# Kernel tuning notes

Measured on AMD Instinct MI355X. Metric: run time of the kernel, lower is better.

The kernel has to match this reference:

```python
import jax, jax.numpy as jnp
import numpy as np

B, C, N = 4, 256, 4096
C4 = C // 4  # q/k projection dim (channels // 4)
BN_EPS = 1e-5


def setup_inputs() -> dict:
    key = jax.random.key(0)
    ks = jax.random.split(key, 4)
    s = 0.05
    return {
        "x": jax.random.normal(ks[0], (B, C, N), jnp.float32),
        # q_conv and k_conv share this weight in the original module
        "wq": jax.random.normal(ks[1], (C4, C), jnp.float32) * s,
        "wv": jax.random.normal(ks[2], (C, C), jnp.float32) * s,
        "bv": jnp.zeros((C,), jnp.float32),
        "wt": jax.random.normal(ks[3], (C, C), jnp.float32) * s,
        "bt": jnp.zeros((C,), jnp.float32),
        "gamma": jnp.ones((C,), jnp.float32),
        "beta": jnp.zeros((C,), jnp.float32),
        "running_mean": jnp.zeros((C,), jnp.float32),
        "running_var": jnp.ones((C,), jnp.float32),
    }


def reference(x, wq, wv, bv, wt, bt, gamma, beta, running_mean, running_var):
    # 1x1 Conv1d == channel matmul. q/k share wq.
    q = jnp.einsum('oc,bcn->bno', wq, x)            # [B, N, C4]
    k = jnp.einsum('oc,bcn->bon', wq, x)            # [B, C4, N]
    energy = jnp.einsum('bno,bom->bnm', q, k)       # [B, N, N]
    attn = jax.nn.softmax(energy, axis=-1)
    # offset-attention L1 re-normalization over dim 1 (query axis)
    attn = attn / (1e-9 + attn.sum(axis=1, keepdims=True))
    v = jnp.einsum('oc,bcn->bon', wv, x) + bv[None, :, None]   # [B, C, N]
    # x_r[b,c,n] = sum_m v[b,c,m] * attn[b,n,m]
    x_r = jnp.einsum('bcm,bnm->bcn', v, attn)       # [B, C, N]
    t = jnp.einsum('oc,bcn->bon', wt, x - x_r) + bt[None, :, None]
    # BatchNorm1d in inference mode (running stats)
    inv = jax.lax.rsqrt(running_var + BN_EPS)
    bn = (t - running_mean[None, :, None]) * (gamma * inv)[None, :, None] + beta[None, :, None]
    return x + jax.nn.relu(bn)
```

## Files before the change

### kernel.cpp

```cpp
#include <hip/hip_runtime.h>
#include <math.h>

namespace {

constexpr int B_ = 4;
constexpr int C_ = 256;
constexpr int C4_ = 64;
constexpr int N_ = 4096;

typedef __attribute__((ext_vector_type(8))) short bf16x8;
typedef __attribute__((ext_vector_type(4))) float f32x4;

__device__ __forceinline__ unsigned short bf16_rne(float f) {
    unsigned u = __float_as_uint(f);
    u += 0x7fffu + ((u >> 16) & 1u);
    return (unsigned short)(u >> 16);
}

__device__ __forceinline__ void g2l16(const unsigned short* g, unsigned short* l) {
    __builtin_amdgcn_global_load_lds(
        (const __attribute__((address_space(1))) unsigned int*)g,
        (__attribute__((address_space(3))) unsigned int*)l, 16, 0, 0);
}

__global__ __launch_bounds__(256) void cvt_kernel(
        const float* __restrict__ wq, const float* __restrict__ wv,
        const float* __restrict__ wt, unsigned short* __restrict__ wcomb,
        unsigned short* __restrict__ wtb) {
    const int i = (blockIdx.x * 256 + threadIdx.x) * 4;
    const float* src;
    unsigned short* dst;
    if (i < 16384) { src = wq + i; dst = wcomb + i; }
    else if (i < 81920) { src = wv + (i - 16384); dst = wcomb + i; }
    else { src = wt + (i - 81920); dst = wtb + (i - 81920); }
    const float4 f = *reinterpret_cast<const float4*>(src);
    ushort4 u;
    u.x = bf16_rne(f.x); u.y = bf16_rne(f.y);
    u.z = bf16_rne(f.z); u.w = bf16_rne(f.w);
    *reinterpret_cast<ushort4*>(dst) = u;
}

__global__ __launch_bounds__(1024, 4) void proj_kernel(
        const float* __restrict__ x, const unsigned short* __restrict__ wcomb,
        const float* __restrict__ bv, unsigned short* __restrict__ qkT,
        unsigned short* __restrict__ v) {
    __shared__ unsigned short xs[2][64][40];
    const int b = blockIdx.y;
    const int n0 = blockIdx.x * 64;
    const int tid = threadIdx.x;
    const int wave = tid >> 6, lane = tid & 63;
    const int ws = wave & 3, oq = wave >> 2;
    const int quad = lane >> 4, l15 = lane & 15;
    const int ca = tid >> 6, na = tid & 63;
    const int cb = (tid + 1024) >> 6, nb2 = (tid + 1024) & 63;
    f32x4 acc[5];
#pragma unroll
    for (int ot = 0; ot < 5; ++ot) acc[ot] = (f32x4){0.f, 0.f, 0.f, 0.f};
    xs[0][na][ca] = bf16_rne(x[((size_t)b * C_ + ca) * N_ + n0 + na]);
    xs[0][nb2][cb] = bf16_rne(x[((size_t)b * C_ + cb) * N_ + n0 + nb2]);
    __syncthreads();
    for (int ch = 0; ch < 8; ++ch) {
        const int buf = ch & 1;
        float la = 0.f, lb = 0.f;
        if (ch < 7) {
            la = x[((size_t)b * C_ + (ch + 1) * 32 + ca) * N_ + n0 + na];
            lb = x[((size_t)b * C_ + (ch + 1) * 32 + cb) * N_ + n0 + nb2];
        }
        const bf16x8 a = *reinterpret_cast<const bf16x8*>(&xs[buf][ws * 16 + l15][quad * 8]);
#pragma unroll
        for (int ot = 0; ot < 5; ++ot) {
            const int gro = oq * 5 + ot;
            const bf16x8 wb = *reinterpret_cast<const bf16x8*>(
                wcomb + (size_t)(gro * 16 + l15) * C_ + ch * 32 + quad * 8);
            acc[ot] = __builtin_amdgcn_mfma_f32_16x16x32_bf16(a, wb, acc[ot], 0, 0, 0);
        }
        if (ch < 7) {
            xs[buf ^ 1][na][ca] = bf16_rne(la);
            xs[buf ^ 1][nb2][cb] = bf16_rne(lb);
        }
        __syncthreads();
    }
    const int n = n0 + ws * 16 + quad * 4;
#pragma unroll
    for (int ot = 0; ot < 5; ++ot) {
        const int gro = oq * 5 + ot;
        if (gro < 4) {
            const int o = gro * 16 + l15;
#pragma unroll
            for (int r = 0; r < 4; ++r)
                qkT[((size_t)b * N_ + n + r) * C4_ + o] = bf16_rne(acc[ot][r]);
        } else {
            const int c = (gro - 4) * 16 + l15;
            const float bb = bv[c];
            ushort4 u;
            u.x = bf16_rne(acc[ot][0] + bb);
            u.y = bf16_rne(acc[ot][1] + bb);
            u.z = bf16_rne(acc[ot][2] + bb);
            u.w = bf16_rne(acc[ot][3] + bb);
            *reinterpret_cast<ushort4*>(&v[((size_t)b * C_ + c) * N_ + n]) = u;
        }
    }
}

__global__ __launch_bounds__(1024, 4) void rowsum_kernel(
        const unsigned short* __restrict__ qkT, float* __restrict__ rowsuminv) {
    __shared__ unsigned short kt[3][64][64];
    __shared__ float red[4][4][16];
    const int gid = blockIdx.x;
    const int xcd = gid & 7;
    const int b = xcd >> 1;
    const int n0 = ((((unsigned)gid >> 3) << 1) | (xcd & 1)) * 64;
    const int tid = threadIdx.x;
    const int wave = tid >> 6, lane = tid & 63;
    const int ws = wave & 3, sg = wave >> 2;
    const int quad = lane >> 4, l15 = lane & 15;
    const unsigned short* qb = qkT + (size_t)b * N_ * C4_;
    const int rowA = lane >> 3;
    const int swc = ((lane & 7) ^ rowA) * 8;
    const int w8 = wave * 8;
    const int r7 = l15 & 7;
    const int c0s = (quad * 8) ^ (r7 << 3);
    const int c1s = (32 + quad * 8) ^ (r7 << 3);
    const unsigned short* qrow = qb + (size_t)(n0 + ws * 16 + l15) * C4_;
    const bf16x8 a0 = *reinterpret_cast<const bf16x8*>(qrow + quad * 8);
    const bf16x8 a1 = *reinterpret_cast<const bf16x8*>(qrow + 32 + quad * 8);
    asm volatile("s_waitcnt vmcnt(0)" ::: "memory");
#define RS_STAGE(sidx, bufS)                                                  \
    if (wave < 8) g2l16(qb + (size_t)((sidx) * 64 + w8 + rowA) * C4_ + swc,   \
                        &kt[bufS][w8][0]);
    RS_STAGE(0, 0);
    RS_STAGE(1, 1);
    if (wave < 8) asm volatile("s_waitcnt vmcnt(1)" ::: "memory");
    __builtin_amdgcn_s_barrier();
    float cs[4] = {};
    int bufR = 0;
#pragma unroll 1
    for (int mt = 0; mt < 64; ++mt) {
        if (mt <= 61) {
            int bufS = bufR + 2; if (bufS >= 3) bufS -= 3;
            RS_STAGE(mt + 2, bufS);
        }
        const bf16x8 kb0 = *reinterpret_cast<const bf16x8*>(&kt[bufR][sg * 16 + l15][c0s]);
        const bf16x8 kb1 = *reinterpret_cast<const bf16x8*>(&kt[bufR][sg * 16 + l15][c1s]);
        __builtin_amdgcn_s_setprio(1);
        f32x4 z = {0.f, 0.f, 0.f, 0.f};
        z = __builtin_amdgcn_mfma_f32_16x16x32_bf16(a0, kb0, z, 0, 0, 0);
        const f32x4 e = __builtin_amdgcn_mfma_f32_16x16x32_bf16(a1, kb1, z, 0, 0, 0);
        __builtin_amdgcn_s_setprio(0);
        cs[0] += __expf(e[0]); cs[1] += __expf(e[1]);
        cs[2] += __expf(e[2]); cs[3] += __expf(e[3]);
        asm volatile("s_waitcnt lgkmcnt(0)" ::: "memory");
        if (wave < 8) {
            if (mt <= 61)      asm volatile("s_waitcnt vmcnt(1)" ::: "memory");
            else if (mt == 62) asm volatile("s_waitcnt vmcnt(0)" ::: "memory");
        }
        __builtin_amdgcn_s_barrier();
        ++bufR; if (bufR >= 3) bufR = 0;
    }
#undef RS_STAGE
#pragma unroll
    for (int r = 0; r < 4; ++r) {
#pragma unroll
        for (int k = 1; k <= 8; k <<= 1) cs[r] += __shfl_xor(cs[r], k, 64);
        if (l15 == 0) red[sg][ws][quad * 4 + r] = cs[r];
    }
    __syncthreads();
    if (tid < 64) {
        const int ws2 = tid >> 4, row = tid & 15;
        const float sum = red[0][ws2][row] + red[1][ws2][row] +
                          red[2][ws2][row] + red[3][ws2][row];
        rowsuminv[(size_t)b * N_ + n0 + ws2 * 16 + row] = 1.0f / sum;
    }
}

__global__ __launch_bounds__(1024, 4) void colsum_kernel(
        const unsigned short* __restrict__ qkT, const float* __restrict__ rowsuminv,
        float* __restrict__ colsuminv) {
    __shared__ float rl[N_];
    __shared__ unsigned short qt[3][64][64];
    __shared__ float red[4][4][16];
    const int gid = blockIdx.x;
    const int xcd = gid & 7;
    const int b = xcd >> 1;
    const int m0 = ((((unsigned)gid >> 3) << 1) | (xcd & 1)) * 64;
    const int tid = threadIdx.x;
    const int wave = tid >> 6, lane = tid & 63;
    const int mw = wave & 3, ng = wave >> 2;
    const int quad = lane >> 4, l15 = lane & 15;
    const unsigned short* qb = qkT + (size_t)b * N_ * C4_;
    const int rowA = lane >> 3;
    const int swc = ((lane & 7) ^ rowA) * 8;
    const int w8 = wave * 8;
    const int r7 = l15 & 7;
    const int c0s = (quad * 8) ^ (r7 << 3);
    const int c1s = (32 + quad * 8) ^ (r7 << 3);
    for (int i = tid; i < N_; i += 1024) rl[i] = rowsuminv[(size_t)b * N_ + i];
    const unsigned short* krow = qb + (size_t)(m0 + mw * 16 + l15) * C4_;
    const bf16x8 kb0 = *reinterpret_cast<const bf16x8*>(krow + quad * 8);
    const bf16x8 kb1 = *reinterpret_cast<const bf16x8*>(krow + 32 + quad * 8);
    asm volatile("s_waitcnt vmcnt(0)" ::: "memory");
#define CS_STAGE(sidx, bufS)                                                  \
    if (wave < 8) g2l16(qb + (size_t)((sidx) * 64 + w8 + rowA) * C4_ + swc,   \
                        &qt[bufS][w8][0]);
    CS_STAGE(0, 0);
    CS_STAGE(1, 1);
    if (wave < 8) asm volatile("s_waitcnt vmcnt(1)" ::: "memory");
    asm volatile("s_waitcnt lgkmcnt(0)" ::: "memory");
    __builtin_amdgcn_s_barrier();
    float cs = 0.f;
    int bufR = 0;
#pragma unroll 1
    for (int nt = 0; nt < 64; ++nt) {
        if (nt <= 61) {
            int bufS = bufR + 2; if (bufS >= 3) bufS -= 3;
            CS_STAGE(nt + 2, bufS);
        }
        const bf16x8 a0 = *reinterpret_cast<const bf16x8*>(&qt[bufR][ng * 16 + l15][c0s]);
        const bf16x8 a1 = *reinterpret_cast<const bf16x8*>(&qt[bufR][ng * 16 + l15][c1s]);
        __builtin_amdgcn_s_setprio(1);
        f32x4 z = {0.f, 0.f, 0.f, 0.f};
        z = __builtin_amdgcn_mfma_f32_16x16x32_bf16(a0, kb0, z, 0, 0, 0);
        const f32x4 e = __builtin_amdgcn_mfma_f32_16x16x32_bf16(a1, kb1, z, 0, 0, 0);
        __builtin_amdgcn_s_setprio(0);
        const int nb = nt * 64 + ng * 16 + quad * 4;
#pragma unroll
        for (int r = 0; r < 4; ++r) cs += __expf(e[r]) * rl[nb + r];
        asm volatile("s_waitcnt lgkmcnt(0)" ::: "memory");
        if (wave < 8) {
            if (nt <= 61)      asm volatile("s_waitcnt vmcnt(1)" ::: "memory");
            else if (nt == 62) asm volatile("s_waitcnt vmcnt(0)" ::: "memory");
        }
        __builtin_amdgcn_s_barrier();
        ++bufR; if (bufR >= 3) bufR = 0;
    }
#undef CS_STAGE
    cs += __shfl_xor(cs, 16, 64);
    cs += __shfl_xor(cs, 32, 64);
    if (quad == 0) red[ng][mw][l15] = cs;
    __syncthreads();
    if (tid < 64) {
        const int mw2 = tid >> 4, l = tid & 15;
        const float sum = red[0][mw2][l] + red[1][mw2][l] +
                          red[2][mw2][l] + red[3][mw2][l];
        colsuminv[(size_t)b * N_ + m0 + mw2 * 16 + l] = 1.0f / (1e-9f + sum);
    }
}

__global__ __launch_bounds__(1024, 4) void final_kernel(
        const float* __restrict__ x, const unsigned short* __restrict__ qkT,
        const unsigned short* __restrict__ v, const unsigned short* __restrict__ wtb,
        const float* __restrict__ rowsuminv, const float* __restrict__ colsuminv,
        const float* __restrict__ bt, const float* __restrict__ gamma,
        const float* __restrict__ beta, const float* __restrict__ rmean,
        const float* __restrict__ rvar, float* __restrict__ out) {
    __shared__ union {
        struct {
            unsigned short vt[3][256][64];
            unsigned short kt[3][64][64];
        } s;
        unsigned short dsm[64][268];
    } u;
    __shared__ unsigned short p_sh[4][16][68];
    __shared__ float ci[N_];
    const int gid = blockIdx.x;
    const int xcd = gid & 7;
    const int b = xcd >> 1;
    const int n0 = ((((unsigned)gid >> 3) << 1) | (xcd & 1)) * 64;
    const int tid = threadIdx.x;
    const int wave = tid >> 6, lane = tid & 63;
    const int ws = wave & 3, g = wave >> 2;
    const int quad = lane >> 4, l15 = lane & 15;
    const unsigned short* qb = qkT + (size_t)b * N_ * C4_;
    const unsigned short* vbg = v + (size_t)b * C_ * N_;
    const int rowA = lane >> 3;
    const int swc = ((lane & 7) ^ rowA) * 8;
    const int w8 = wave * 8;
    const int r7 = l15 & 7;
    const int c0s = (quad * 8) ^ (r7 << 3);
    const int c1s = (32 + quad * 8) ^ (r7 << 3);
    const unsigned short* qrow = qb + (size_t)(n0 + ws * 16 + l15) * C4_;
    const bf16x8 q0 = *reinterpret_cast<const bf16x8*>(qrow + quad * 8);
    const bf16x8 q1 = *reinterpret_cast<const bf16x8*>(qrow + 32 + quad * 8);
    const float rli = rowsuminv[(size_t)b * N_ + n0 + ws * 16 + l15];
    {
        const float4 c4 = *reinterpret_cast<const float4*>(colsuminv + (size_t)b * N_ + tid * 4);
        *reinterpret_cast<float4*>(&ci[tid * 4]) = c4;
    }
    asm volatile("s_waitcnt vmcnt(0)" ::: "memory");
#define STAGE_TILE(sidx, bufS)                                                          \
    do {                                                                                \
        g2l16(vbg + (size_t)(w8 + rowA) * N_ + (sidx) * 64 + swc,                       \
              &u.s.vt[bufS][w8][0]);                                                    \
        g2l16(vbg + (size_t)(w8 + 128 + rowA) * N_ + (sidx) * 64 + swc,                 \
              &u.s.vt[bufS][w8 + 128][0]);                                              \
        if (wave < 8)                                                                   \
            g2l16(qb + (size_t)((sidx) * 64 + w8 + rowA) * C4_ + swc,                   \
                  &u.s.kt[bufS][w8][0]);                                                \
    } while (0)
    STAGE_TILE(0, 0);
    STAGE_TILE(1, 1);
    if (wave < 8) asm volatile("s_waitcnt vmcnt(3)" ::: "memory");
    else          asm volatile("s_waitcnt vmcnt(2)" ::: "memory");
    asm volatile("s_waitcnt lgkmcnt(0)" ::: "memory");
    __builtin_amdgcn_s_barrier();
    f32x4 acc[4];
#pragma unroll
    for (int j = 0; j < 4; ++j) acc[j] = (f32x4){0.f, 0.f, 0.f, 0.f};
    int bufR = 0;
#pragma unroll 1
    for (int t = 0; t < 64; ++t) {
        if (t <= 61) {
            int bufS = bufR + 2; if (bufS >= 3) bufS -= 3;
            STAGE_TILE(t + 2, bufS);
        }
        {
            const unsigned short(*ktb)[64] = u.s.kt[bufR];
            const bf16x8 ka0 = *reinterpret_cast<const bf16x8*>(&ktb[g * 16 + l15][c0s]);
            const bf16x8 ka1 = *reinterpret_cast<const bf16x8*>(&ktb[g * 16 + l15][c1s]);
            __builtin_amdgcn_s_setprio(1);
            f32x4 z = {0.f, 0.f, 0.f, 0.f};
            z = __builtin_amdgcn_mfma_f32_16x16x32_bf16(ka0, q0, z, 0, 0, 0);
            z = __builtin_amdgcn_mfma_f32_16x16x32_bf16(ka1, q1, z, 0, 0, 0);
            __builtin_amdgcn_s_setprio(0);
            const float4 civ = *reinterpret_cast<const float4*>(&ci[t * 64 + g * 16 + quad * 4]);
            ushort4 pk;
            pk.x = bf16_rne(__expf(z[0]) * rli * civ.x);
            pk.y = bf16_rne(__expf(z[1]) * rli * civ.y);
            pk.z = bf16_rne(__expf(z[2]) * rli * civ.z);
            pk.w = bf16_rne(__expf(z[3]) * rli * civ.w);
            *reinterpret_cast<ushort4*>(&p_sh[ws][l15][g * 16 + quad * 4]) = pk;
        }
        asm volatile("s_waitcnt lgkmcnt(0)" ::: "memory");
        __builtin_amdgcn_s_barrier();
        {
            const bf16x8 pa0 = *reinterpret_cast<const bf16x8*>(&p_sh[ws][l15][quad * 8]);
            const bf16x8 pa1 = *reinterpret_cast<const bf16x8*>(&p_sh[ws][l15][32 + quad * 8]);
            const unsigned short(*vtb)[64] = u.s.vt[bufR];
            __builtin_amdgcn_s_setprio(1);
#pragma unroll
            for (int j = 0; j < 4; ++j) {
                const int vr = (g * 4 + j) * 16 + l15;
                const bf16x8 vb0 = *reinterpret_cast<const bf16x8*>(&vtb[vr][c0s]);
                const bf16x8 vb1 = *reinterpret_cast<const bf16x8*>(&vtb[vr][c1s]);
                acc[j] = __builtin_amdgcn_mfma_f32_16x16x32_bf16(pa0, vb0, acc[j], 0, 0, 0);
                acc[j] = __builtin_amdgcn_mfma_f32_16x16x32_bf16(pa1, vb1, acc[j], 0, 0, 0);
            }
            __builtin_amdgcn_s_setprio(0);
        }
        asm volatile("s_waitcnt lgkmcnt(0)" ::: "memory");
        if (t <= 61) {
            if (wave < 8) asm volatile("s_waitcnt vmcnt(3)" ::: "memory");
            else          asm volatile("s_waitcnt vmcnt(2)" ::: "memory");
        } else {
            asm volatile("s_waitcnt vmcnt(0)" ::: "memory");
        }
        __builtin_amdgcn_s_barrier();
        ++bufR; if (bufR >= 3) bufR = 0;
    }
#undef STAGE_TILE
#pragma unroll
    for (int j = 0; j < 4; ++j) {
        const int c = (g * 4 + j) * 16 + l15;
        const float4 xv = *reinterpret_cast<const float4*>(
            &x[((size_t)b * C_ + c) * N_ + n0 + ws * 16 + quad * 4]);
        const float xvr[4] = {xv.x, xv.y, xv.z, xv.w};
#pragma unroll
        for (int r = 0; r < 4; ++r)
            u.dsm[ws * 16 + quad * 4 + r][c] = bf16_rne(xvr[r] - acc[j][r]);
    }
    __syncthreads();
    bf16x8 da[8];
#pragma unroll
    for (int k = 0; k < 8; ++k)
        da[k] = *reinterpret_cast<const bf16x8*>(&u.dsm[ws * 16 + l15][k * 32 + quad * 8]);
    f32x4 tacc[4];
#pragma unroll
    for (int j = 0; j < 4; ++j) tacc[j] = (f32x4){0.f, 0.f, 0.f, 0.f};
#pragma unroll
    for (int j = 0; j < 4; ++j) {
        const int ot = g * 4 + j;
#pragma unroll
        for (int k = 0; k < 8; ++k) {
            const bf16x8 wb = *reinterpret_cast<const bf16x8*>(
                wtb + (size_t)(ot * 16 + l15) * C_ + k * 32 + quad * 8);
            tacc[j] = __builtin_amdgcn_mfma_f32_16x16x32_bf16(da[k], wb, tacc[j], 0, 0, 0);
        }
    }
#pragma unroll
    for (int j = 0; j < 4; ++j) {
        const int o = (g * 4 + j) * 16 + l15;
        const float gg = gamma[o] * rsqrtf(rvar[o] + 1e-5f);
        const float mn = rmean[o], bbet = beta[o], bo = bt[o];
        const size_t oi = ((size_t)b * C_ + o) * N_ + n0 + ws * 16 + quad * 4;
        const float4 xo = *reinterpret_cast<const float4*>(&x[oi]);
        float4 res;
        res.x = xo.x + fmaxf((tacc[j][0] + bo - mn) * gg + bbet, 0.f);
        res.y = xo.y + fmaxf((tacc[j][1] + bo - mn) * gg + bbet, 0.f);
        res.z = xo.z + fmaxf((tacc[j][2] + bo - mn) * gg + bbet, 0.f);
        res.w = xo.w + fmaxf((tacc[j][3] + bo - mn) * gg + bbet, 0.f);
        *reinterpret_cast<float4*>(&out[oi]) = res;
    }
}

}

extern "C" void kernel_launch(void* const* d_in, const int* in_sizes, int n_in,
                              void* d_out, int out_size, void* d_ws, size_t ws_size,
                              hipStream_t stream) {
    const float* x = (const float*)d_in[0];
    const float* wq = (const float*)d_in[1];
    const float* wv = (const float*)d_in[2];
    const float* bv = (const float*)d_in[3];
    const float* wt = (const float*)d_in[4];
    const float* bt = (const float*)d_in[5];
    const float* gamma = (const float*)d_in[6];
    const float* beta = (const float*)d_in[7];
    const float* rmean = (const float*)d_in[8];
    const float* rvar = (const float*)d_in[9];
    float* out = (float*)d_out;

    char* base = (char*)d_ws;
    unsigned short* qkT = (unsigned short*)base;
    unsigned short* vw = (unsigned short*)(base + (2u << 20));
    unsigned short* wtb = (unsigned short*)(base + (10u << 20));
    unsigned short* wcomb = (unsigned short*)(base + (10u << 20) + (128u << 10));
    float* rowsuminv = (float*)(base + (10u << 20) + (288u << 10));
    float* colsuminv = (float*)(base + (10u << 20) + (352u << 10));

    cvt_kernel<<<dim3(144), dim3(256), 0, stream>>>(wq, wv, wt, wcomb, wtb);
    proj_kernel<<<dim3(N_ / 64, B_), dim3(1024), 0, stream>>>(x, wcomb, bv, qkT, vw);
    rowsum_kernel<<<dim3(N_ / 64 * B_), dim3(1024), 0, stream>>>(qkT, rowsuminv);
    colsum_kernel<<<dim3(N_ / 64 * B_), dim3(1024), 0, stream>>>(qkT, rowsuminv, colsuminv);
    final_kernel<<<dim3(N_ / 64 * B_), dim3(1024), 0, stream>>>(
        x, qkT, vw, wtb, rowsuminv, colsuminv, bt, gamma, beta, rmean, rvar, out);
}
```

Before: 260.0 us.

## Use 32x32x16 MFMA and 256-row K tiles in rowsum/colsum kernels

Reworks the rowsum and colsum kernels so each wave computes a 32x32 energy tile with 32x32x16 bf16 MFMAs over a 256-row staged tile per iteration. All 16 waves now issue async global-to-LDS loads, and the loop runs 16 iterations instead of 64. This cuts barrier and loop overhead per unit of work and uses larger MFMA shapes. In exchange it takes more LDS (a triple buffer of 256x64 bf16) and more registers (16-float accumulators), which may lower occupancy. The reduction index remapping for the 32x32 output layout adds some correctness risk.

```diff
diff --git a/kernel.cpp b/kernel.cpp
--- a/kernel.cpp
+++ b/kernel.cpp
@@ -10,6 +10,7 @@
 
 typedef __attribute__((ext_vector_type(8))) short bf16x8;
 typedef __attribute__((ext_vector_type(4))) float f32x4;
+typedef __attribute__((ext_vector_type(16))) float f32x16;
 
 __device__ __forceinline__ unsigned short bf16_rne(float f) {
     unsigned u = __float_as_uint(f);
@@ -104,72 +105,82 @@
 
 __global__ __launch_bounds__(1024, 4) void rowsum_kernel(
         const unsigned short* __restrict__ qkT, float* __restrict__ rowsuminv) {
-    __shared__ unsigned short kt[3][64][64];
-    __shared__ float red[4][4][16];
+    __shared__ unsigned short kt[3][256][64];
+    __shared__ float red[2][8][2][16];
     const int gid = blockIdx.x;
     const int xcd = gid & 7;
     const int b = xcd >> 1;
     const int n0 = ((((unsigned)gid >> 3) << 1) | (xcd & 1)) * 64;
     const int tid = threadIdx.x;
     const int wave = tid >> 6, lane = tid & 63;
-    const int ws = wave & 3, sg = wave >> 2;
-    const int quad = lane >> 4, l15 = lane & 15;
+    const int nt = wave >> 3, ms = wave & 7;
+    const int l31 = lane & 31, h = lane >> 5;
     const unsigned short* qb = qkT + (size_t)b * N_ * C4_;
     const int rowA = lane >> 3;
     const int swc = ((lane & 7) ^ rowA) * 8;
-    const int w8 = wave * 8;
-    const int r7 = l15 & 7;
-    const int c0s = (quad * 8) ^ (r7 << 3);
-    const int c1s = (32 + quad * 8) ^ (r7 << 3);
-    const unsigned short* qrow = qb + (size_t)(n0 + ws * 16 + l15) * C4_;
-    const bf16x8 a0 = *reinterpret_cast<const bf16x8*>(qrow + quad * 8);
-    const bf16x8 a1 = *reinterpret_cast<const bf16x8*>(qrow + 32 + quad * 8);
+    const int w16 = wave * 16;
+    const int r7 = l31 & 7;
+    const unsigned short* qrow = qb + (size_t)(n0 + nt * 32 + l31) * C4_ + h * 8;
+    bf16x8 qa[4];
+#pragma unroll
+    for (int j = 0; j < 4; ++j)
+        qa[j] = *reinterpret_cast<const bf16x8*>(qrow + j * 16);
     asm volatile("s_waitcnt vmcnt(0)" ::: "memory");
 #define RS_STAGE(sidx, bufS)                                                  \
-    if (wave < 8) g2l16(qb + (size_t)((sidx) * 64 + w8 + rowA) * C4_ + swc,   \
-                        &kt[bufS][w8][0]);
+    do {                                                                      \
+        g2l16(qb + (size_t)((sidx) * 256 + w16 + rowA) * C4_ + swc,           \
+              &kt[bufS][w16][0]);                                             \
+        g2l16(qb + (size_t)((sidx) * 256 + w16 + 8 + rowA) * C4_ + swc,       \
+              &kt[bufS][w16 + 8][0]);                                         \
+    } while (0)
     RS_STAGE(0, 0);
     RS_STAGE(1, 1);
-    if (wave < 8) asm volatile("s_waitcnt vmcnt(1)" ::: "memory");
+    asm volatile("s_waitcnt vmcnt(2)" ::: "memory");
     __builtin_amdgcn_s_barrier();
-    float cs[4] = {};
+    f32x16 acc = (f32x16){0.f, 0.f, 0.f, 0.f, 0.f, 0.f, 0.f, 0.f,
+                          0.f, 0.f, 0.f, 0.f, 0.f, 0.f, 0.f, 0.f};
     int bufR = 0;
 #pragma unroll 1
-    for (int mt = 0; mt < 64; ++mt) {
-        if (mt <= 61) {
+    for (int t = 0; t < 16; ++t) {
+        if (t <= 13) {
             int bufS = bufR + 2; if (bufS >= 3) bufS -= 3;
-            RS_STAGE(mt + 2, bufS);
-        }
-        const bf16x8 kb0 = *reinterpret_cast<const bf16x8*>(&kt[bufR][sg * 16 + l15][c0s]);
-        const bf16x8 kb1 = *reinterpret_cast<const bf16x8*>(&kt[bufR][sg * 16 + l15][c1s]);
+            RS_STAGE(t + 2, bufS);
+        }
+        f32x16 z = (f32x16){0.f, 0.f, 0.f, 0.f, 0.f, 0.f, 0.f, 0.f,
+                            0.f, 0.f, 0.f, 0.f, 0.f, 0.f, 0.f, 0.f};
         __builtin_amdgcn_s_setprio(1);
-        f32x4 z = {0.f, 0.f, 0.f, 0.f};
-        z = __builtin_amdgcn_mfma_f32_16x16x32_bf16(a0, kb0, z, 0, 0, 0);
-        const f32x4 e = __builtin_amdgcn_mfma_f32_16x16x32_bf16(a1, kb1, z, 0, 0, 0);
+#pragma unroll
+        for (int j = 0; j < 4; ++j) {
+            const bf16x8 kb = *reinterpret_cast<const bf16x8*>(
+                &kt[bufR][ms * 32 + l31][(j * 16 + h * 8) ^ (r7 << 3)]);
+            z = __builtin_amdgcn_mfma_f32_32x32x16_bf16(qa[j], kb, z, 0, 0, 0);
+        }
         __builtin_amdgcn_s_setprio(0);
-        cs[0] += __expf(e[0]); cs[1] += __expf(e[1]);
-        cs[2] += __expf(e[2]); cs[3] += __expf(e[3]);
+#pragma unroll
+        for (int r = 0; r < 16; ++r) acc[r] += __expf(z[r]);
         asm volatile("s_waitcnt lgkmcnt(0)" ::: "memory");
-        if (wave < 8) {
-            if (mt <= 61)      asm volatile("s_waitcnt vmcnt(1)" ::: "memory");
-            else if (mt == 62) asm volatile("s_waitcnt vmcnt(0)" ::: "memory");
-        }
+        if (t <= 13)      asm volatile("s_waitcnt vmcnt(2)" ::: "memory");
+        else if (t == 14) asm volatile("s_waitcnt vmcnt(0)" ::: "memory");
         __builtin_amdgcn_s_barrier();
         ++bufR; if (bufR >= 3) bufR = 0;
     }
 #undef RS_STAGE
 #pragma unroll
-    for (int r = 0; r < 4; ++r) {
-#pragma unroll
-        for (int k = 1; k <= 8; k <<= 1) cs[r] += __shfl_xor(cs[r], k, 64);
-        if (l15 == 0) red[sg][ws][quad * 4 + r] = cs[r];
+    for (int r = 0; r < 16; ++r) {
+        float s = acc[r];
+#pragma unroll
+        for (int k = 1; k <= 16; k <<= 1) s += __shfl_xor(s, k, 64);
+        if (l31 == 0) red[nt][ms][h][r] = s;
     }
     __syncthreads();
     if (tid < 64) {
-        const int ws2 = tid >> 4, row = tid & 15;
-        const float sum = red[0][ws2][row] + red[1][ws2][row] +
-                          red[2][ws2][row] + red[3][ws2][row];
-        rowsuminv[(size_t)b * N_ + n0 + ws2 * 16 + row] = 1.0f / sum;
+        const int v = tid & 31, nt2 = tid >> 5;
+        const int reg = (v & 3) | ((v >> 3) << 2);
+        const int hh = (v >> 2) & 1;
+        float sum = 0.f;
+#pragma unroll
+        for (int m = 0; m < 8; ++m) sum += red[nt2][m][hh][reg];
+        rowsuminv[(size_t)b * N_ + n0 + nt2 * 32 + v] = 1.0f / sum;
     }
 }
 
@@ -177,72 +188,78 @@
         const unsigned short* __restrict__ qkT, const float* __restrict__ rowsuminv,
         float* __restrict__ colsuminv) {
     __shared__ float rl[N_];
-    __shared__ unsigned short qt[3][64][64];
-    __shared__ float red[4][4][16];
+    __shared__ unsigned short qt[3][256][64];
+    __shared__ float red2[8][2][32];
     const int gid = blockIdx.x;
     const int xcd = gid & 7;
     const int b = xcd >> 1;
     const int m0 = ((((unsigned)gid >> 3) << 1) | (xcd & 1)) * 64;
     const int tid = threadIdx.x;
     const int wave = tid >> 6, lane = tid & 63;
-    const int mw = wave & 3, ng = wave >> 2;
-    const int quad = lane >> 4, l15 = lane & 15;
+    const int ms2 = wave >> 3, ns = wave & 7;
+    const int l31 = lane & 31, h = lane >> 5;
     const unsigned short* qb = qkT + (size_t)b * N_ * C4_;
     const int rowA = lane >> 3;
     const int swc = ((lane & 7) ^ rowA) * 8;
-    const int w8 = wave * 8;
-    const int r7 = l15 & 7;
-    const int c0s = (quad * 8) ^ (r7 << 3);
-    const int c1s = (32 + quad * 8) ^ (r7 << 3);
+    const int w16 = wave * 16;
+    const int r7 = l31 & 7;
     for (int i = tid; i < N_; i += 1024) rl[i] = rowsuminv[(size_t)b * N_ + i];
-    const unsigned short* krow = qb + (size_t)(m0 + mw * 16 + l15) * C4_;
-    const bf16x8 kb0 = *reinterpret_cast<const bf16x8*>(krow + quad * 8);
-    const bf16x8 kb1 = *reinterpret_cast<const bf16x8*>(krow + 32 + quad * 8);
+    const unsigned short* krow = qb + (size_t)(m0 + ms2 * 32 + l31) * C4_ + h * 8;
+    bf16x8 kbf[4];
+#pragma unroll
+    for (int j = 0; j < 4; ++j)
+        kbf[j] = *reinterpret_cast<const bf16x8*>(krow + j * 16);
     asm volatile("s_waitcnt vmcnt(0)" ::: "memory");
 #define CS_STAGE(sidx, bufS)                                                  \
-    if (wave < 8) g2l16(qb + (size_t)((sidx) * 64 + w8 + rowA) * C4_ + swc,   \
-                        &qt[bufS][w8][0]);
+    do {                                                                      \
+        g2l16(qb + (size_t)((sidx) * 256 + w16 + rowA) * C4_ + swc,           \
+              &qt[bufS][w16][0]);                                             \
+        g2l16(qb + (size_t)((sidx) * 256 + w16 + 8 + rowA) * C4_ + swc,       \
+              &qt[bufS][w16 + 8][0]);                                         \
+    } while (0)
     CS_STAGE(0, 0);
     CS_STAGE(1, 1);
-    if (wave < 8) asm volatile("s_waitcnt vmcnt(1)" ::: "memory");
+    asm volatile("s_waitcnt vmcnt(2)" ::: "memory");
     asm volatile("s_waitcnt lgkmcnt(0)" ::: "memory");
     __builtin_amdgcn_s_barrier();
-    float cs = 0.f;
+    float csa = 0.f;
     int bufR = 0;
 #pragma unroll 1
-    for (int nt = 0; nt < 64; ++nt) {
-        if (nt <= 61) {
+    for (int t = 0; t < 16; ++t) {
+        if (t <= 13) {
             int bufS = bufR + 2; if (bufS >= 3) bufS -= 3;
-            CS_STAGE(nt + 2, bufS);
-        }
-        const bf16x8 a0 = *reinterpret_cast<const bf16x8*>(&qt[bufR][ng * 16 + l15][c0s]);
-        const bf16x8 a1 = *reinterpret_cast<const bf16x8*>(&qt[bufR][ng * 16 + l15][c1s]);
+            CS_STAGE(t + 2, bufS);
+        }
+        f32x16 z = (f32x16){0.f, 0.f, 0.f, 0.f, 0.f, 0.f, 0.f, 0.f,
+                            0.f, 0.f, 0.f, 0.f, 0.f, 0.f, 0.f, 0.f};
         __builtin_amdgcn_s_setprio(1);
-        f32x4 z = {0.f, 0.f, 0.f, 0.f};
-        z = __builtin_amdgcn_mfma_f32_16x16x32_bf16(a0, kb0, z, 0, 0, 0);
-        const f32x4 e = __builtin_amdgcn_mfma_f32_16x16x32_bf16(a1, kb1, z, 0, 0, 0);
+#pragma unroll
+        for (int j = 0; j < 4; ++j) {
+            const bf16x8 qa = *reinterpret_cast<const bf16x8*>(
+                &qt[bufR][ns * 32 + l31][(j * 16 + h * 8) ^ (r7 << 3)]);
+            z = __builtin_amdgcn_mfma_f32_32x32x16_bf16(qa, kbf[j], z, 0, 0, 0);
+        }
         __builtin_amdgcn_s_setprio(0);
-        const int nb = nt * 64 + ng * 16 + quad * 4;
-#pragma unroll
-        for (int r = 0; r < 4; ++r) cs += __expf(e[r]) * rl[nb + r];
+        const int nb = t * 256 + ns * 32 + 4 * h;
+#pragma unroll
+        for (int r = 0; r < 16; ++r)
+            csa += __expf(z[r]) * rl[nb + (r & 3) + 8 * (r >> 2)];
         asm volatile("s_waitcnt lgkmcnt(0)" ::: "memory");
-        if (wave < 8) {
-            if (nt <= 61)      asm volatile("s_waitcnt vmcnt(1)" ::: "memory");
-            else if (nt == 62) asm volatile("s_waitcnt vmcnt(0)" ::: "memory");
-        }
+        if (t <= 13)      asm volatile("s_waitcnt vmcnt(2)" ::: "memory");
+        else if (t == 14) asm volatile("s_waitcnt vmcnt(0)" ::: "memory");
         __builtin_amdgcn_s_barrier();
         ++bufR; if (bufR >= 3) bufR = 0;
     }
 #undef CS_STAGE
-    cs += __shfl_xor(cs, 16, 64);
-    cs += __shfl_xor(cs, 32, 64);
-    if (quad == 0) red[ng][mw][l15] = cs;
+    csa += __shfl_xor(csa, 32, 64);
+    if (h == 0) red2[ns][ms2][l31] = csa;
     __syncthreads();
     if (tid < 64) {
-        const int mw2 = tid >> 4, l = tid & 15;
-        const float sum = red[0][mw2][l] + red[1][mw2][l] +
-                          red[2][mw2][l] + red[3][mw2][l];
-        colsuminv[(size_t)b * N_ + m0 + mw2 * 16 + l] = 1.0f / (1e-9f + sum);
+        const int ml = tid & 31, mg = tid >> 5;
+        float sum = 0.f;
+#pragma unroll
+        for (int n = 0; n < 8; ++n) sum += red2[n][mg][ml];
+        colsuminv[(size_t)b * N_ + m0 + mg * 32 + ml] = 1.0f / (1e-9f + sum);
     }
 }
 
```

After: 257.2 us. No clear change (-1.1%).
